# Kernel optimization log

Hardware: AMD Instinct MI355X
Metric: run time of the kernel (lower is better)

Reference implementation:

```python
import jax, jax.numpy as jnp
import numpy as np

BITS = 4
OFF = 8          # 2**(BITS-1)
QLEVELS = 15.0   # 2**BITS - 1
IN_F, OUT_F, FP_F, TOKENS = 4096, 4096, 256, 4096
INT_F = IN_F - FP_F


def unpack_i4(w_packed):
    """Invert pack_to_i4: packed uint8 col k holds signed int4 cols (2k: low nibble, 2k+1: high)."""
    lo = (w_packed & 0x0F).astype(jnp.int8)
    hi = ((w_packed >> 4) & 0x0F).astype(jnp.int8)
    lo = jnp.where(lo >= 8, lo - 16, lo)
    hi = jnp.where(hi >= 8, hi - 16, hi)
    return jnp.stack([lo, hi], axis=-1).reshape(w_packed.shape[0], -1)  # (out, int_features)


def setup_inputs() -> dict:
    key = jax.random.key(0)
    k1, k2, k3, k4, k5 = jax.random.split(key, 5)
    x = jax.random.normal(k1, (1, TOKENS, IN_F), dtype=jnp.float16)
    perm = jax.random.permutation(k2, IN_F)
    fp_indices = jnp.sort(perm[:FP_F]).astype(jnp.int64)
    int_indices = jnp.sort(perm[FP_F:]).astype(jnp.int64)
    # signed int4 weight values in [-8, 7], packed two-per-byte like pack_to_i4
    w_vals = jax.random.randint(k3, (OUT_F, INT_F), -8, 8, dtype=jnp.int8)
    u = (w_vals.astype(jnp.int32) & 0x0F).astype(jnp.uint8)
    int_weight = (u[:, 0::2] | (u[:, 1::2] << 4)).astype(jnp.uint8)  # (out, INT_F//2)
    weights_scales = (jax.random.uniform(k4, (OUT_F, 1)) * 0.01 + 1e-3).astype(jnp.float16)
    # reduced_w = row-sum of the dequantized int-column weights (as in from_float)
    reduced_w = (w_vals.astype(jnp.float32).sum(axis=1, keepdims=True)
                 * weights_scales.astype(jnp.float32)).T.astype(jnp.float16)  # (1, out)
    fp_weight = (jax.random.normal(k5, (OUT_F, FP_F)) * 0.02).astype(jnp.float16)
    bias = jnp.zeros((OUT_F,), dtype=jnp.float16)
    return {"x": x, "int_weight": int_weight, "weights_scales": weights_scales,
            "reduced_w": reduced_w, "fp_weight": fp_weight, "bias": bias,
            "int_indices": int_indices, "fp_indices": fp_indices}


def reference(x, int_weight, weights_scales, reduced_w, fp_weight, bias,
              int_indices, fp_indices):
    x2 = x[0]                                   # (M, in_features)
    int_x = x2[:, int_indices].astype(jnp.float32)   # (M, INT_F)
    fp_x = x2[:, fp_indices].astype(jnp.float32)     # (M, FP_F)
    # asymmetric per-row quantization to signed int4
    mn = int_x.min(axis=1, keepdims=True)
    mx = int_x.max(axis=1, keepdims=True)
    scale = jnp.maximum((mx - mn) / QLEVELS, 1e-8)   # (M,1)
    zero = mn                                        # (M,1)
    q = jnp.clip(jnp.round((int_x - zero) / scale) - OFF, -8, 7).astype(jnp.int8)
    w_int = unpack_i4(int_weight)                    # (out, INT_F) int8
    int_result = jnp.matmul(q.astype(jnp.int32), w_int.T.astype(jnp.int32))  # (M, out) int32
    fp_result = fp_x @ fp_weight.T.astype(jnp.float32) + bias.astype(jnp.float32)
    # asym dequant: x ~ (q + OFF)*scale + zero, W = w_int * w_scale, sum_j W_j = reduced_w
    w_scale = weights_scales.astype(jnp.float32)[:, 0][None, :]   # (1, out)
    out = (scale * w_scale * int_result.astype(jnp.float32)
           + (zero + scale * OFF) * reduced_w.astype(jnp.float32)
           + fp_result)
    return out.astype(jnp.float16)[None]             # (1, M, out)
```

## Files before the change

### kernel.cpp

```cpp
#include <hip/hip_runtime.h>
#include <hip/hip_bf16.h>

#define IN_FEAT 4096
#define OUT_FEAT 4096
#define FP_FEAT 256
#define INT_FEAT 3840
#define TOKENS 4096
#define PACKED_W (INT_FEAT / 2)

#define NT_I8 60
#define NT_ALL 68

typedef __attribute__((ext_vector_type(8))) short short8;
typedef __attribute__((ext_vector_type(4))) float f32x4;
typedef __attribute__((ext_vector_type(4))) int   int32x4;

#define AQ8_OFF   0u
#define WB8_OFF   16777216u
#define AFP_OFF   33554432u
#define WFP_OFF   35651584u
#define SCALE_OFF 37748736u
#define ZERO_OFF  37765120u
#define WS_NEED   37781504u

__global__ __launch_bounds__(256) void prep_kernel(
    const float* __restrict__ x,
    const int* __restrict__ int_idx_raw,
    const int* __restrict__ fp_idx_raw,
    const int* __restrict__ wpacked_raw,
    const float* __restrict__ fpw,
    const float* __restrict__ wscale,
    signed char* __restrict__ Aq8,
    __hip_bfloat16* __restrict__ Afp,
    signed char* __restrict__ Wb8,
    __hip_bfloat16* __restrict__ Wfp,
    float* __restrict__ scale_ws,
    float* __restrict__ zero_ws)
{
    const int t = threadIdx.x;
    if (blockIdx.x < TOKENS) {
        const int m = blockIdx.x;
        const float* xr = x + (size_t)m * IN_FEAT;
        const bool is64 = (int_idx_raw[1] == 0) && (int_idx_raw[3] == 0);

        float v[15];
        float mn = 1e30f, mx = -1e30f;
#pragma unroll
        for (int j = 0; j < 15; ++j) {
            int k = t + j * 256;
            int idx = is64 ? int_idx_raw[2 * k] : int_idx_raw[k];
            float f = xr[idx];
            v[j] = f;
            mn = fminf(mn, f);
            mx = fmaxf(mx, f);
        }
#pragma unroll
        for (int off = 1; off < 64; off <<= 1) {
            mn = fminf(mn, __shfl_xor(mn, off));
            mx = fmaxf(mx, __shfl_xor(mx, off));
        }
        __shared__ float smn[4], smx[4];
        int wid = t >> 6, lane = t & 63;
        if (lane == 0) { smn[wid] = mn; smx[wid] = mx; }
        __syncthreads();
        if (t == 0) {
            float rmn = fminf(fminf(smn[0], smn[1]), fminf(smn[2], smn[3]));
            float rmx = fmaxf(fmaxf(smx[0], smx[1]), fmaxf(smx[2], smx[3]));
            float sc = fmaxf((rmx - rmn) / 15.0f, 1e-8f);
            smn[0] = rmn;
            smx[0] = sc;
            scale_ws[m] = sc;
            zero_ws[m] = rmn;
        }
        __syncthreads();
        const float zero = smn[0];
        const float sc = smx[0];

        signed char* ar = Aq8 + (size_t)m * INT_FEAT;
#pragma unroll
        for (int j = 0; j < 15; ++j) {
            int k = t + j * 256;
            float q = rintf((v[j] - zero) / sc) - 8.0f;
            q = fminf(fmaxf(q, -8.0f), 7.0f);
            ar[k] = (signed char)(int)q;
        }
        int fpi = is64 ? fp_idx_raw[2 * t] : fp_idx_raw[t];
        Afp[(size_t)m * FP_FEAT + t] = __float2bfloat16(xr[fpi] / sc);
    } else {
        const int n = blockIdx.x - TOKENS;
        bool is_i32 = true;
#pragma unroll
        for (int j = 0; j < 8; ++j) {
            unsigned w = (unsigned)wpacked_raw[j];
            if (w > 0xFFu) is_i32 = false;
        }
        short* wo = (short*)(Wb8 + (size_t)n * INT_FEAT);
#pragma unroll
        for (int j = 0; j < 8; ++j) {
            int k = t + j * 256;
            if (k < PACKED_W) {
                int p = is_i32 ? wpacked_raw[(size_t)n * PACKED_W + k]
                               : ((const unsigned char*)wpacked_raw)[(size_t)n * PACKED_W + k];
                int lo = p & 15; if (lo >= 8) lo -= 16;
                int hi = (p >> 4) & 15; if (hi >= 8) hi -= 16;
                wo[k] = (short)(((unsigned char)lo) | ((unsigned short)(unsigned char)hi << 8));
            }
        }
        float wsn = wscale[n];
        Wfp[(size_t)n * FP_FEAT + t] = __float2bfloat16(fpw[(size_t)n * FP_FEAT + t] / wsn);
    }
}


#define PREFETCH(VT, AN, BN)                                                   \
    {                                                                          \
        const int pbB = ((VT) & 3) << 15;                                      \
        _Pragma("unroll")                                                      \
        for (int nf = 0; nf < 4; ++nf)                                         \
            BN[nf] = *(const int32x4*)(lds + pbB + bOff[nf]);                  \
        _Pragma("unroll")                                                      \
        for (int mf = 0; mf < 8; ++mf)                                         \
            AN[mf] = *(const int32x4*)(lds + pbB + aOff[mf]);                  \
    }

#define MFMA_I8(AC, BC)                                                        \
    _Pragma("unroll")                                                          \
    for (int mf = 0; mf < 8; ++mf)                                             \
        _Pragma("unroll")                                                      \
        for (int nf = 0; nf < 4; ++nf)                                         \
            acc[mf][nf] = __builtin_amdgcn_mfma_i32_16x16x64_i8(               \
                AC[mf], BC[nf], acc[mf][nf], 0, 0, 0);

#define MFMA_BF(AC, BC)                                                        \
    _Pragma("unroll")                                                          \
    for (int mf = 0; mf < 8; ++mf)                                             \
        _Pragma("unroll")                                                      \
        for (int nf = 0; nf < 4; ++nf)                                         \
            acc[mf][nf] = __builtin_bit_cast(int32x4,                          \
                __builtin_amdgcn_mfma_f32_16x16x32_bf16(                       \
                    __builtin_bit_cast(short8, AC[mf]),                        \
                    __builtin_bit_cast(short8, BC[nf]),                        \
                    __builtin_bit_cast(f32x4, acc[mf][nf]), 0, 0, 0));

#define ENDBAR4()                                                              \
    asm volatile("s_waitcnt vmcnt(4)" ::: "memory");                           \
    __builtin_amdgcn_sched_barrier(0);                                         \
    __builtin_amdgcn_s_barrier();                                              \
    __builtin_amdgcn_sched_barrier(0);

#define ENDBAR0()                                                              \
    asm volatile("s_waitcnt vmcnt(0)" ::: "memory");                           \
    __builtin_amdgcn_sched_barrier(0);                                         \
    __builtin_amdgcn_s_barrier();                                              \
    __builtin_amdgcn_sched_barrier(0);

#define ENDBARN()                                                              \
    __builtin_amdgcn_sched_barrier(0);                                         \
    __builtin_amdgcn_s_barrier();                                              \
    __builtin_amdgcn_sched_barrier(0);

__global__ __launch_bounds__(512, 2) void gemm256_i8(
    const signed char* __restrict__ Aq8,
    const __hip_bfloat16* __restrict__ Afp,
    const signed char* __restrict__ Wb8,
    const __hip_bfloat16* __restrict__ Wfp,
    const float* __restrict__ scale_ws,
    const float* __restrict__ zero_ws,
    const float* __restrict__ wscale,
    const float* __restrict__ reduced,
    const float* __restrict__ bias,
    float* __restrict__ out)
{
    __shared__ __align__(16) char lds[131072];

    const int t = threadIdx.x;
    const int lane = t & 63, wid = t >> 6;
    const int wr = wid >> 2;
    const int wc = wid & 3;
    const int r16 = lane & 15;
    const int kg = lane >> 4;

    const int bid = blockIdx.x;
    const int sb = (bid & 7) * 32 + (bid >> 3);
    const int tileM = (sb >> 4) * 256;
    const int tileN = (sb & 15) * 256;

    const int id0 = t, id1 = 512 + t;
    const int r0 = id0 >> 2, c0 = id0 & 3;
    const int r1 = id1 >> 2, c1 = id1 & 3;
    const int sw0 = ((c0 ^ ((r0 >> 1) & 3)) << 4);
    const int sw1 = ((c1 ^ ((r1 >> 1) & 3)) << 4);
    const char* a8_0 = (const char*)Aq8 + (size_t)(tileM + r0) * INT_FEAT + sw0;
    const char* a8_1 = (const char*)Aq8 + (size_t)(tileM + r1) * INT_FEAT + sw1;
    const char* b8_0 = (const char*)Wb8 + (size_t)(tileN + r0) * INT_FEAT + sw0;
    const char* b8_1 = (const char*)Wb8 + (size_t)(tileN + r1) * INT_FEAT + sw1;
    const char* af_0 = (const char*)Afp + (size_t)(tileM + r0) * 512 + sw0;
    const char* af_1 = (const char*)Afp + (size_t)(tileM + r1) * 512 + sw1;
    const char* bf_0 = (const char*)Wfp + (size_t)(tileN + r0) * 512 + sw0;
    const char* bf_1 = (const char*)Wfp + (size_t)(tileN + r1) * 512 + sw1;
    const int dst0 = id0 << 4, dst1 = id1 << 4;

    auto stage = [&](int vt, int bufB) {
        const bool i8p = vt < NT_I8;
        const int ko = i8p ? vt * 64 : (vt - NT_I8) * 64;
        const char* pa0 = (i8p ? a8_0 : af_0) + ko;
        const char* pa1 = (i8p ? a8_1 : af_1) + ko;
        const char* pb0 = (i8p ? b8_0 : bf_0) + ko;
        const char* pb1 = (i8p ? b8_1 : bf_1) + ko;
        __builtin_amdgcn_global_load_lds(
            (const __attribute__((address_space(1))) void*)pa0,
            (__attribute__((address_space(3))) void*)(lds + bufB + dst0), 16, 0, 0);
        __builtin_amdgcn_global_load_lds(
            (const __attribute__((address_space(1))) void*)pa1,
            (__attribute__((address_space(3))) void*)(lds + bufB + dst1), 16, 0, 0);
        __builtin_amdgcn_global_load_lds(
            (const __attribute__((address_space(1))) void*)pb0,
            (__attribute__((address_space(3))) void*)(lds + bufB + 16384 + dst0), 16, 0, 0);
        __builtin_amdgcn_global_load_lds(
            (const __attribute__((address_space(1))) void*)pb1,
            (__attribute__((address_space(3))) void*)(lds + bufB + 16384 + dst1), 16, 0, 0);
    };

    int aOff[8], bOff[4];
#pragma unroll
    for (int mf = 0; mf < 8; ++mf) {
        int ra = wr * 128 + mf * 16 + r16;
        aOff[mf] = ra * 64 + ((((ra >> 1) & 3) ^ kg) << 4);
    }
#pragma unroll
    for (int nf = 0; nf < 4; ++nf) {
        int rb = wc * 64 + nf * 16 + r16;
        bOff[nf] = 16384 + rb * 64 + ((((rb >> 1) & 3) ^ kg) << 4);
    }

    int32x4 acc[8][4];
#pragma unroll
    for (int mf = 0; mf < 8; ++mf)
#pragma unroll
        for (int nf = 0; nf < 4; ++nf)
            acc[mf][nf] = (int32x4){0, 0, 0, 0};

    int32x4 aP[8], bP[4], aN[8], bN[4];

    stage(0, 0);
    stage(1, 32768);
    stage(2, 65536);
    asm volatile("s_waitcnt vmcnt(4)" ::: "memory");
    __builtin_amdgcn_sched_barrier(0);
    __builtin_amdgcn_s_barrier();
    __builtin_amdgcn_sched_barrier(0);
    PREFETCH(0, aP, bP);

    for (int vt = 0; vt < NT_I8 - 2; vt += 2) {
        PREFETCH(vt + 1, aN, bN);
        stage(vt + 3, ((vt + 3) & 3) << 15);
        MFMA_I8(aP, bP);
        ENDBAR4();

        PREFETCH(vt + 2, aP, bP);
        stage(vt + 4, ((vt + 4) & 3) << 15);
        MFMA_I8(aN, bN);
        ENDBAR4();
    }

    PREFETCH(59, aN, bN);
    stage(61, (61 & 3) << 15);
    MFMA_I8(aP, bP);
    ENDBAR4();

    PREFETCH(60, aP, bP);
    stage(62, (62 & 3) << 15);
    MFMA_I8(aN, bN);
    ENDBAR4();

#pragma unroll
    for (int mf = 0; mf < 8; ++mf)
#pragma unroll
        for (int nf = 0; nf < 4; ++nf) {
            int32x4 vi = acc[mf][nf];
            f32x4 vf;
#pragma unroll
            for (int i = 0; i < 4; ++i) vf[i] = (float)vi[i];
            acc[mf][nf] = __builtin_bit_cast(int32x4, vf);
        }

    PREFETCH(61, aN, bN); stage(63, (63 & 3) << 15); MFMA_BF(aP, bP); ENDBAR4();
    PREFETCH(62, aP, bP); stage(64, (64 & 3) << 15); MFMA_BF(aN, bN); ENDBAR4();
    PREFETCH(63, aN, bN); stage(65, (65 & 3) << 15); MFMA_BF(aP, bP); ENDBAR4();
    PREFETCH(64, aP, bP); stage(66, (66 & 3) << 15); MFMA_BF(aN, bN); ENDBAR4();
    PREFETCH(65, aN, bN); stage(67, (67 & 3) << 15); MFMA_BF(aP, bP); ENDBAR4();
    PREFETCH(66, aP, bP);                            MFMA_BF(aN, bN); ENDBAR0();
    PREFETCH(67, aN, bN);                            MFMA_BF(aP, bP); ENDBARN();
    MFMA_BF(aN, bN);

    const int cr4 = kg * 4;
#pragma unroll
    for (int mf = 0; mf < 8; ++mf) {
#pragma unroll
        for (int nf = 0; nf < 4; ++nf) {
            int n = tileN + wc * 64 + nf * 16 + r16;
            float ws = wscale[n];
            float rd = reduced[n];
            float bs = bias[n];
            f32x4 av = __builtin_bit_cast(f32x4, acc[mf][nf]);
#pragma unroll
            for (int i = 0; i < 4; ++i) {
                int m = tileM + wr * 128 + mf * 16 + cr4 + i;
                float sc = scale_ws[m];
                float zr = zero_ws[m];
                out[(size_t)m * OUT_FEAT + n] =
                    sc * ws * av[i]
                    + (zr + sc * 8.0f) * rd + bs;
            }
        }
    }
}

extern "C" void kernel_launch(void* const* d_in, const int* in_sizes, int n_in,
                              void* d_out, int out_size, void* d_ws, size_t ws_size,
                              hipStream_t stream)
{
    const void* px = 0; const void* pw = 0; const void* pfpw = 0;
    const void* pii = 0; const void* pfi = 0;
    const void* p4096[3] = {0, 0, 0}; int n4096 = 0;
    for (int i = 0; i < n_in; ++i) {
        switch (in_sizes[i]) {
            case 16777216: px = d_in[i]; break;
            case 7864320:  pw = d_in[i]; break;
            case 1048576:  pfpw = d_in[i]; break;
            case 3840:     pii = d_in[i]; break;
            case 256:      pfi = d_in[i]; break;
            case 4096:     if (n4096 < 3) p4096[n4096++] = d_in[i]; break;
            default: break;
        }
    }
    if (!px || !pw || !pfpw || !pii || !pfi || n4096 != 3) return;

    const float* x       = (const float*)px;
    const int*   wpacked = (const int*)pw;
    const float* wscale  = (const float*)p4096[0];
    const float* reduced = (const float*)p4096[1];
    const float* bias    = (const float*)p4096[2];
    const float* fpw     = (const float*)pfpw;
    const int*   int_idx = (const int*)pii;
    const int*   fp_idx  = (const int*)pfi;
    float*       out     = (float*)d_out;

    if (ws_size < (size_t)WS_NEED) return;

    char* ws = (char*)d_ws;
    signed char*    Aq8 = (signed char*)(ws + AQ8_OFF);
    signed char*    Wb8 = (signed char*)(ws + WB8_OFF);
    __hip_bfloat16* Afp = (__hip_bfloat16*)(ws + AFP_OFF);
    __hip_bfloat16* Wfp = (__hip_bfloat16*)(ws + WFP_OFF);
    float* scale_ws     = (float*)(ws + SCALE_OFF);
    float* zero_ws      = (float*)(ws + ZERO_OFF);

    prep_kernel<<<TOKENS + OUT_FEAT, 256, 0, stream>>>(
        x, int_idx, fp_idx, wpacked, fpw, wscale,
        Aq8, Afp, Wb8, Wfp, scale_ws, zero_ws);
    gemm256_i8<<<256, 512, 0, stream>>>(Aq8, Afp, Wb8, Wfp,
                                        scale_ws, zero_ws,
                                        wscale, reduced, bias, out);
}
```

Before: 96.53 us.

## Switch GEMM inner loop from 16x16 to 32x32 MFMA tiles

Replaces the 16x16x64 i8 and 16x16x32 bf16 MFMA instructions with 32x32x32 i8 and 32x32x16 bf16 variants. Each warp now covers its 128x64 output with 4x2 larger fragments split into two k-substeps, with new LDS offset and swizzle math and a 32x32 output layout in the epilogue. It also adds a partial lgkmcnt wait so MFMAs can begin before all LDS reads for the stage have landed. The aim is fewer fragment loads per MFMA and higher MFMA throughput, at the cost of a more complex register layout and possible LDS bank-conflict changes.

```diff
diff --git a/kernel.cpp b/kernel.cpp
--- a/kernel.cpp
+++ b/kernel.cpp
@@ -11,9 +11,11 @@
 #define NT_I8 60
 #define NT_ALL 68
 
-typedef __attribute__((ext_vector_type(8))) short short8;
-typedef __attribute__((ext_vector_type(4))) float f32x4;
-typedef __attribute__((ext_vector_type(4))) int   int32x4;
+typedef __attribute__((ext_vector_type(8)))  short short8;
+typedef __attribute__((ext_vector_type(4)))  float f32x4;
+typedef __attribute__((ext_vector_type(4)))  int   int32x4;
+typedef __attribute__((ext_vector_type(16))) int   int32x16;
+typedef __attribute__((ext_vector_type(16))) float f32x16;
 
 #define AQ8_OFF   0u
 #define WB8_OFF   16777216u
@@ -116,31 +118,43 @@
     {                                                                          \
         const int pbB = ((VT) & 3) << 15;                                      \
         _Pragma("unroll")                                                      \
-        for (int nf = 0; nf < 4; ++nf)                                         \
-            BN[nf] = *(const int32x4*)(lds + pbB + bOff[nf]);                  \
+        for (int nf = 0; nf < 2; ++nf)                                         \
+            _Pragma("unroll")                                                  \
+            for (int ks = 0; ks < 2; ++ks)                                     \
+                BN[nf][ks] = *(const int32x4*)(lds + pbB + bOff[nf][ks]);      \
         _Pragma("unroll")                                                      \
-        for (int mf = 0; mf < 8; ++mf)                                         \
-            AN[mf] = *(const int32x4*)(lds + pbB + aOff[mf]);                  \
-    }
+        for (int mf = 0; mf < 4; ++mf)                                         \
+            _Pragma("unroll")                                                  \
+            for (int ks = 0; ks < 2; ++ks)                                     \
+                AN[mf][ks] = *(const int32x4*)(lds + pbB + aOff[mf][ks]);      \
+    }
+
+#define WAIT12()                                                               \
+    asm volatile("s_waitcnt lgkmcnt(12)" ::: "memory");                        \
+    __builtin_amdgcn_sched_barrier(0);
 
 #define MFMA_I8(AC, BC)                                                        \
     _Pragma("unroll")                                                          \
-    for (int mf = 0; mf < 8; ++mf)                                             \
+    for (int ks = 0; ks < 2; ++ks)                                             \
         _Pragma("unroll")                                                      \
-        for (int nf = 0; nf < 4; ++nf)                                         \
-            acc[mf][nf] = __builtin_amdgcn_mfma_i32_16x16x64_i8(               \
-                AC[mf], BC[nf], acc[mf][nf], 0, 0, 0);
+        for (int mf = 0; mf < 4; ++mf)                                         \
+            _Pragma("unroll")                                                  \
+            for (int nf = 0; nf < 2; ++nf)                                     \
+                acc[mf][nf] = __builtin_amdgcn_mfma_i32_32x32x32_i8(           \
+                    AC[mf][ks], BC[nf][ks], acc[mf][nf], 0, 0, 0);
 
 #define MFMA_BF(AC, BC)                                                        \
     _Pragma("unroll")                                                          \
-    for (int mf = 0; mf < 8; ++mf)                                             \
+    for (int ks = 0; ks < 2; ++ks)                                             \
         _Pragma("unroll")                                                      \
-        for (int nf = 0; nf < 4; ++nf)                                         \
-            acc[mf][nf] = __builtin_bit_cast(int32x4,                          \
-                __builtin_amdgcn_mfma_f32_16x16x32_bf16(                       \
-                    __builtin_bit_cast(short8, AC[mf]),                        \
-                    __builtin_bit_cast(short8, BC[nf]),                        \
-                    __builtin_bit_cast(f32x4, acc[mf][nf]), 0, 0, 0));
+        for (int mf = 0; mf < 4; ++mf)                                         \
+            _Pragma("unroll")                                                  \
+            for (int nf = 0; nf < 2; ++nf)                                     \
+                acc[mf][nf] = __builtin_bit_cast(int32x16,                     \
+                    __builtin_amdgcn_mfma_f32_32x32x16_bf16(                   \
+                        __builtin_bit_cast(short8, AC[mf][ks]),                \
+                        __builtin_bit_cast(short8, BC[nf][ks]),                \
+                        __builtin_bit_cast(f32x16, acc[mf][nf]), 0, 0, 0));
 
 #define ENDBAR4()                                                              \
     asm volatile("s_waitcnt vmcnt(4)" ::: "memory");                           \
@@ -177,8 +191,8 @@
     const int lane = t & 63, wid = t >> 6;
     const int wr = wid >> 2;
     const int wc = wid & 3;
-    const int r16 = lane & 15;
-    const int kg = lane >> 4;
+    const int r32 = lane & 31;
+    const int kg2 = lane >> 5;
 
     const int bid = blockIdx.x;
     const int sb = (bid & 7) * 32 + (bid >> 3);
@@ -221,26 +235,34 @@
             (__attribute__((address_space(3))) void*)(lds + bufB + 16384 + dst1), 16, 0, 0);
     };
 
-    int aOff[8], bOff[4];
-#pragma unroll
-    for (int mf = 0; mf < 8; ++mf) {
-        int ra = wr * 128 + mf * 16 + r16;
-        aOff[mf] = ra * 64 + ((((ra >> 1) & 3) ^ kg) << 4);
-    }
-#pragma unroll
-    for (int nf = 0; nf < 4; ++nf) {
-        int rb = wc * 64 + nf * 16 + r16;
-        bOff[nf] = 16384 + rb * 64 + ((((rb >> 1) & 3) ^ kg) << 4);
-    }
-
-    int32x4 acc[8][4];
-#pragma unroll
-    for (int mf = 0; mf < 8; ++mf)
-#pragma unroll
-        for (int nf = 0; nf < 4; ++nf)
-            acc[mf][nf] = (int32x4){0, 0, 0, 0};
-
-    int32x4 aP[8], bP[4], aN[8], bN[4];
+    int aOff[4][2], bOff[2][2];
+#pragma unroll
+    for (int mf = 0; mf < 4; ++mf)
+#pragma unroll
+        for (int ks = 0; ks < 2; ++ks) {
+            int ra = wr * 128 + mf * 32 + r32;
+            int q = ks * 2 + kg2;
+            aOff[mf][ks] = ra * 64 + (((q ^ ((ra >> 1) & 3))) << 4);
+        }
+#pragma unroll
+    for (int nf = 0; nf < 2; ++nf)
+#pragma unroll
+        for (int ks = 0; ks < 2; ++ks) {
+            int rb = wc * 64 + nf * 32 + r32;
+            int q = ks * 2 + kg2;
+            bOff[nf][ks] = 16384 + rb * 64 + (((q ^ ((rb >> 1) & 3))) << 4);
+        }
+
+    int32x16 acc[4][2];
+#pragma unroll
+    for (int mf = 0; mf < 4; ++mf)
+#pragma unroll
+        for (int nf = 0; nf < 2; ++nf)
+#pragma unroll
+            for (int i = 0; i < 16; ++i)
+                acc[mf][nf][i] = 0;
+
+    int32x4 aP[4][2], bP[2][2], aN[4][2], bN[2][2];
 
     stage(0, 0);
     stage(1, 32768);
@@ -254,62 +276,66 @@
     for (int vt = 0; vt < NT_I8 - 2; vt += 2) {
         PREFETCH(vt + 1, aN, bN);
         stage(vt + 3, ((vt + 3) & 3) << 15);
+        WAIT12();
         MFMA_I8(aP, bP);
         ENDBAR4();
 
         PREFETCH(vt + 2, aP, bP);
         stage(vt + 4, ((vt + 4) & 3) << 15);
+        WAIT12();
         MFMA_I8(aN, bN);
         ENDBAR4();
     }
 
     PREFETCH(59, aN, bN);
     stage(61, (61 & 3) << 15);
+    WAIT12();
     MFMA_I8(aP, bP);
     ENDBAR4();
 
     PREFETCH(60, aP, bP);
     stage(62, (62 & 3) << 15);
+    WAIT12();
     MFMA_I8(aN, bN);
     ENDBAR4();
 
 #pragma unroll
-    for (int mf = 0; mf < 8; ++mf)
-#pragma unroll
-        for (int nf = 0; nf < 4; ++nf) {
-            int32x4 vi = acc[mf][nf];
-            f32x4 vf;
-#pragma unroll
-            for (int i = 0; i < 4; ++i) vf[i] = (float)vi[i];
-            acc[mf][nf] = __builtin_bit_cast(int32x4, vf);
-        }
-
-    PREFETCH(61, aN, bN); stage(63, (63 & 3) << 15); MFMA_BF(aP, bP); ENDBAR4();
-    PREFETCH(62, aP, bP); stage(64, (64 & 3) << 15); MFMA_BF(aN, bN); ENDBAR4();
-    PREFETCH(63, aN, bN); stage(65, (65 & 3) << 15); MFMA_BF(aP, bP); ENDBAR4();
-    PREFETCH(64, aP, bP); stage(66, (66 & 3) << 15); MFMA_BF(aN, bN); ENDBAR4();
-    PREFETCH(65, aN, bN); stage(67, (67 & 3) << 15); MFMA_BF(aP, bP); ENDBAR4();
-    PREFETCH(66, aP, bP);                            MFMA_BF(aN, bN); ENDBAR0();
-    PREFETCH(67, aN, bN);                            MFMA_BF(aP, bP); ENDBARN();
+    for (int mf = 0; mf < 4; ++mf)
+#pragma unroll
+        for (int nf = 0; nf < 2; ++nf) {
+            int32x16 vi = acc[mf][nf];
+            f32x16 vf;
+#pragma unroll
+            for (int i = 0; i < 16; ++i) vf[i] = (float)vi[i];
+            acc[mf][nf] = __builtin_bit_cast(int32x16, vf);
+        }
+
+    PREFETCH(61, aN, bN); stage(63, (63 & 3) << 15); WAIT12(); MFMA_BF(aP, bP); ENDBAR4();
+    PREFETCH(62, aP, bP); stage(64, (64 & 3) << 15); WAIT12(); MFMA_BF(aN, bN); ENDBAR4();
+    PREFETCH(63, aN, bN); stage(65, (65 & 3) << 15); WAIT12(); MFMA_BF(aP, bP); ENDBAR4();
+    PREFETCH(64, aP, bP); stage(66, (66 & 3) << 15); WAIT12(); MFMA_BF(aN, bN); ENDBAR4();
+    PREFETCH(65, aN, bN); stage(67, (67 & 3) << 15); WAIT12(); MFMA_BF(aP, bP); ENDBAR4();
+    PREFETCH(66, aP, bP);                            WAIT12(); MFMA_BF(aN, bN); ENDBAR0();
+    PREFETCH(67, aN, bN);                            WAIT12(); MFMA_BF(aP, bP); ENDBARN();
     MFMA_BF(aN, bN);
 
-    const int cr4 = kg * 4;
-#pragma unroll
-    for (int mf = 0; mf < 8; ++mf) {
-#pragma unroll
-        for (int nf = 0; nf < 4; ++nf) {
-            int n = tileN + wc * 64 + nf * 16 + r16;
+#pragma unroll
+    for (int mf = 0; mf < 4; ++mf) {
+#pragma unroll
+        for (int nf = 0; nf < 2; ++nf) {
+            int n = tileN + wc * 64 + nf * 32 + r32;
             float ws = wscale[n];
             float rd = reduced[n];
             float bs = bias[n];
-            f32x4 av = __builtin_bit_cast(f32x4, acc[mf][nf]);
-#pragma unroll
-            for (int i = 0; i < 4; ++i) {
-                int m = tileM + wr * 128 + mf * 16 + cr4 + i;
+            f32x16 av = __builtin_bit_cast(f32x16, acc[mf][nf]);
+#pragma unroll
+            for (int reg = 0; reg < 16; ++reg) {
+                int row = (reg & 3) + 8 * (reg >> 2) + 4 * kg2;
+                int m = tileM + wr * 128 + mf * 32 + row;
                 float sc = scale_ws[m];
                 float zr = zero_ws[m];
                 out[(size_t)m * OUT_FEAT + n] =
-                    sc * ws * av[i]
+                    sc * ws * av[reg]
                     + (zr + sc * 8.0f) * rd + bs;
             }
         }
```

After: 127.3 us. +31.8%, slower.
